# Optimization experiments

Measured on AMD Instinct MI355X. Metric: run time of the kernel, lower is better.

Reference implementation:

```python
import jax, jax.numpy as jnp
import numpy as np

NUM_FEAT = 64
K = 3  # dynamic kernel size
B, T, H, W = 1, 10, 192, 192


def _conv3x3(x, w, b):
    # x: [B,Cin,H,W], w: [Cout,Cin,3,3], b: [Cout]
    y = jax.lax.conv_general_dilated(x, w, window_strides=(1, 1), padding='SAME',
                                     dimension_numbers=('NCHW', 'OIHW', 'NCHW'))
    return y + b[None, :, None, None]


def _lrelu(x):
    return jnp.where(x >= 0, x, 0.1 * x)


def _kernel_conv(feat, core):
    # Per-pixel dynamic 3x3 filtering (CDVD-TSPNL KernelConv, sep_conv=False, no bias, N=1).
    # feat: [B,C,H,W], core: [B, K*K*C, H, W] -> out: [B,C,H,W]
    b, c, h, w = feat.shape
    pad = jnp.pad(feat, ((0, 0), (0, 0), (1, 1), (1, 1)))
    # 9 shifted copies, kernel-index kk = i*K + j matches core.view(b,1,K*K,c,h,w) layout
    stack = jnp.stack([pad[:, :, i:i + h, j:j + w] for i in range(K) for j in range(K)], axis=1)  # [B,9,C,H,W]
    core = core.reshape(b, K * K, c, h, w)
    return jnp.sum(core * stack, axis=1)  # sum over kernel taps; mean over N=1 frames is identity


def setup_inputs() -> dict:
    key = jax.random.key(0)
    ks = jax.random.split(key, 8)
    s = 0.02  # keep recurrent magnitudes stable
    nf = NUM_FEAT
    return {
        'feature': jax.random.normal(ks[0], (B, T, nf, H, W), jnp.float32),
        'w_kc1': jax.random.normal(ks[1], (nf, 2 * nf, 3, 3), jnp.float32) * s,
        'b_kc1': jnp.zeros((nf,), jnp.float32),
        'w_kc2': jax.random.normal(ks[2], (K * K * nf, nf, 3, 3), jnp.float32) * s,
        'b_kc2': jnp.zeros((K * K * nf,), jnp.float32),
        'w_c1': jax.random.normal(ks[3], (2 * nf, 2 * nf, 3, 3), jnp.float32) * s,
        'b_c1': jnp.zeros((2 * nf,), jnp.float32),
        'w_c2': jax.random.normal(ks[4], (nf, nf, 3, 3), jnp.float32) * s,
        'b_c2': jnp.zeros((nf,), jnp.float32),
        'w_c3': jax.random.normal(ks[5], (nf, nf, 3, 3), jnp.float32) * s,
        'b_c3': jnp.zeros((nf,), jnp.float32),
    }


def reference(feature, w_kc1, b_kc1, w_kc2, b_kc2, w_c1, b_c1, w_c2, b_c2, w_c3, b_c3):
    b, t, c, h, w = feature.shape
    feat_prop = feature[:, t - 1]  # [B,C,H,W]
    outs = [feat_prop]
    for i in range(t - 2, -1, -1):
        x_feat = feature[:, i]
        feat_concat = jnp.concatenate([x_feat, feat_prop], axis=1)
        kernel_predict = _conv3x3(_lrelu(_conv3x3(feat_concat, w_kc1, b_kc1)), w_kc2, b_kc2)
        feat_prop = _kernel_conv(feat_prop, kernel_predict)
        feat_fusion = _lrelu(_conv3x3(jnp.concatenate([x_feat, feat_prop], axis=1), w_c1, b_c1))
        p1, p2 = feat_fusion[:, :c], feat_fusion[:, c:]
        p1 = p1 * jax.nn.sigmoid(_conv3x3(p1, w_c2, b_c2))
        p2 = p2 * jax.nn.sigmoid(_conv3x3(p2, w_c3, b_c3))
        feat_prop = p1 + p2
        outs.append(feat_prop)
    return jnp.stack(outs[::-1], axis=1)  # [B,T,C,H,W]
```

## Files before the change

kernel.cpp:

```cpp
#include <hip/hip_runtime.h>

#define HH 192
#define WW 192
#define PW 194
#define HWSZ (HH*WW)
#define PHW (PW*PW)
#define CHW (64*HWSZ)

typedef __attribute__((ext_vector_type(8))) short bf16x8;
typedef __attribute__((ext_vector_type(4))) short bf16x4;
typedef __attribute__((ext_vector_type(4))) float f32x4;
typedef __attribute__((ext_vector_type(4))) unsigned int u32x4;

typedef __attribute__((address_space(3))) void as3_void;
typedef __attribute__((address_space(1))) const void as1_cvoid;

__device__ __forceinline__ float bf2f(short h) {
    union { unsigned u; float f; } c; c.u = ((unsigned)(unsigned short)h) << 16; return c.f;
}
__device__ __forceinline__ short f2bf(float f) {
    union { float f; unsigned u; } c; c.f = f;
    unsigned u = c.u;
    return (short)((u + 0x7FFFu + ((u >> 16) & 1u)) >> 16);
}
__device__ __forceinline__ float sigm(float v) {
    return 1.f / (1.f + __expf(-v));
}

template<int COUT>
__device__ __forceinline__ void stagew(short* lds, const short* wt, int kb, int mt,
                                       int tid, int wv)
{
    const short* wbase = wt + ((size_t)(kb*9)*COUT + mt*64)*64;
#pragma unroll
    for (int i = 0; i < 18; ++i) {
        int q = i*256 + tid;
        const short* gp = wbase + (size_t)(q >> 9)*COUT*64 + (q & 511)*8;
        __builtin_amdgcn_global_load_lds((as1_cvoid*)gp,
            (as3_void*)(lds + (i*256 + wv*64)*8), 16, 0, 0);
    }
}

template<int KB, int COUT>
__global__ __launch_bounds__(256, 2)
void convk(const short* __restrict__ in0, int cs0, int cb0,
           const short* __restrict__ in1, int cs1, int cb1,
           const short* __restrict__ wt, const float* __restrict__ bias,
           short* __restrict__ outb, int pado, int rowW, int cdst, int lrelu)
{
    __shared__ __align__(16) short lds[9*64*64];
    const int tid = threadIdx.x;
    const int l  = tid & 63, wv = tid >> 6;
    const int lr = l & 15,  lg = l >> 4;
    const int y  = blockIdx.x % HH;
    const int mt = blockIdx.x / HH;

    f32x4 acc[4][3];
#pragma unroll
    for (int a = 0; a < 4; ++a)
#pragma unroll
        for (int b = 0; b < 3; ++b) acc[a][b] = f32x4{0.f,0.f,0.f,0.f};

#pragma unroll 1
    for (int kb = 0; kb < KB; ++kb) {
        const short* src = (kb == 0) ? in0 : in1;
        const int cs = (kb == 0) ? cs0 : cs1;
        const int cb = (kb == 0) ? cb0 : cb1;
        if (kb) __syncthreads();
        stagew<COUT>(lds, wt, kb, mt, tid, wv);
        __syncthreads();
#pragma unroll
        for (int dy = 0; dy < 3; ++dy)
#pragma unroll
        for (int dx = 0; dx < 3; ++dx) {
            const int tap = dy*3 + dx;
#pragma unroll
            for (int ks = 0; ks < 2; ++ks) {
                bf16x8 bv[3];
#pragma unroll
                for (int nf = 0; nf < 3; ++nf) {
                    int px = wv*48 + nf*16 + lr + dx;
                    bv[nf] = *reinterpret_cast<const bf16x8*>(
                        src + (size_t)((y+dy)*PW + px)*cs + cb + ks*32 + lg*8);
                }
                const int s = ks*4 + lg;
#pragma unroll
                for (int mf = 0; mf < 4; ++mf) {
                    int row = mf*16 + lr;
                    bf16x8 av = *reinterpret_cast<const bf16x8*>(
                        &lds[(tap*64 + row)*64 + ((s ^ (row & 7))*8)]);
                    acc[mf][0] = __builtin_amdgcn_mfma_f32_16x16x32_bf16(av, bv[0], acc[mf][0], 0,0,0);
                    acc[mf][1] = __builtin_amdgcn_mfma_f32_16x16x32_bf16(av, bv[1], acc[mf][1], 0,0,0);
                    acc[mf][2] = __builtin_amdgcn_mfma_f32_16x16x32_bf16(av, bv[2], acc[mf][2], 0,0,0);
                }
            }
        }
    }

#pragma unroll
    for (int mf = 0; mf < 4; ++mf) {
        const int coutb = mt*64 + mf*16 + lg*4;
        f32x4 bv = *reinterpret_cast<const f32x4*>(bias + coutb);
#pragma unroll
        for (int nf = 0; nf < 3; ++nf) {
            const int x = wv*48 + nf*16 + lr;
            bf16x4 pk;
#pragma unroll
            for (int j = 0; j < 4; ++j) {
                float t = acc[mf][nf][j] + bv[j];
                if (lrelu) t = (t >= 0.f) ? t : 0.1f*t;
                pk[j] = f2bf(t);
            }
            *reinterpret_cast<bf16x4*>(outb + (size_t)((y+pado)*rowW + (x+pado))*cdst + coutb) = pk;
        }
    }
}

__global__ __launch_bounds__(256, 2)
void gatek(const short* __restrict__ fus, const short* __restrict__ wg,
           const float* __restrict__ b2, const float* __restrict__ b3,
           float* __restrict__ dml, short* __restrict__ fpst)
{
    __shared__ __align__(16) short lds[9*64*64];
    const int tid = threadIdx.x;
    const int l  = tid & 63, wv = tid >> 6;
    const int lr = l & 15,  lg = l >> 4;
    const int y  = blockIdx.x;

    f32x4 acc1[4][3], acc2[4][3];
#pragma unroll
    for (int a = 0; a < 4; ++a)
#pragma unroll
        for (int b = 0; b < 3; ++b) { acc1[a][b] = f32x4{0.f,0.f,0.f,0.f}; acc2[a][b] = f32x4{0.f,0.f,0.f,0.f}; }

#pragma unroll 1
    for (int g = 0; g < 2; ++g) {
        if (g) __syncthreads();
        stagew<64>(lds, wg + (size_t)g*9*64*64, 0, 0, tid, wv);
        __syncthreads();
#pragma unroll
        for (int dy = 0; dy < 3; ++dy)
#pragma unroll
        for (int dx = 0; dx < 3; ++dx) {
            const int tap = dy*3 + dx;
#pragma unroll
            for (int ks = 0; ks < 2; ++ks) {
                bf16x8 bv[3];
#pragma unroll
                for (int nf = 0; nf < 3; ++nf) {
                    int px = wv*48 + nf*16 + lr + dx;
                    bv[nf] = *reinterpret_cast<const bf16x8*>(
                        fus + (size_t)((y+dy)*PW + px)*128 + g*64 + ks*32 + lg*8);
                }
                const int s = ks*4 + lg;
#pragma unroll
                for (int mf = 0; mf < 4; ++mf) {
                    int row = mf*16 + lr;
                    bf16x8 av = *reinterpret_cast<const bf16x8*>(
                        &lds[(tap*64 + row)*64 + ((s ^ (row & 7))*8)]);
                    f32x4* ac = g ? &acc2[mf][0] : &acc1[mf][0];
                    ac[0] = __builtin_amdgcn_mfma_f32_16x16x32_bf16(av, bv[0], ac[0], 0,0,0);
                    ac[1] = __builtin_amdgcn_mfma_f32_16x16x32_bf16(av, bv[1], ac[1], 0,0,0);
                    ac[2] = __builtin_amdgcn_mfma_f32_16x16x32_bf16(av, bv[2], ac[2], 0,0,0);
                }
            }
        }
    }

#pragma unroll
    for (int mf = 0; mf < 4; ++mf) {
        const int c = mf*16 + lg*4;
        f32x4 v2 = *reinterpret_cast<const f32x4*>(b2 + c);
        f32x4 v3 = *reinterpret_cast<const f32x4*>(b3 + c);
#pragma unroll
        for (int nf = 0; nf < 3; ++nf) {
            const int x = wv*48 + nf*16 + lr;
            bf16x4 p1 = *reinterpret_cast<const bf16x4*>(fus + (size_t)((y+1)*PW + (x+1))*128 + c);
            bf16x4 p2 = *reinterpret_cast<const bf16x4*>(fus + (size_t)((y+1)*PW + (x+1))*128 + 64 + c);
            bf16x4 pk;
#pragma unroll
            for (int j = 0; j < 4; ++j) {
                float r = bf2f(p1[j]) * sigm(acc1[mf][nf][j] + v2[j])
                        + bf2f(p2[j]) * sigm(acc2[mf][nf][j] + v3[j]);
                dml[(size_t)(c + j)*HWSZ + y*WW + x] = r;
                pk[j] = f2bf(r);
            }
            *reinterpret_cast<bf16x4*>(fpst + (size_t)((y+1)*PW + (x+1))*64 + c) = pk;
        }
    }
}

__global__ __launch_bounds__(256)
void kconvk(const short* __restrict__ kp, const short* __restrict__ fp,
            short* __restrict__ outp)
{
    int t  = blockIdx.x*256 + threadIdx.x;
    int cg = t & 7, pix = t >> 3;
    int y = pix / WW, x = pix - y*WW;
    float acc[8];
#pragma unroll
    for (int e = 0; e < 8; ++e) acc[e] = 0.f;
    const short* kpp = kp + (size_t)pix*576 + cg*8;
#pragma unroll
    for (int tap = 0; tap < 9; ++tap) {
        int dy = tap / 3, dx = tap - dy*3;
        bf16x8 kv = *reinterpret_cast<const bf16x8*>(kpp + tap*64);
        bf16x8 fv = *reinterpret_cast<const bf16x8*>(fp + (size_t)((y+dy)*PW + (x+dx))*64 + cg*8);
#pragma unroll
        for (int e = 0; e < 8; ++e) acc[e] += bf2f(kv[e]) * bf2f(fv[e]);
    }
    bf16x8 o;
#pragma unroll
    for (int e = 0; e < 8; ++e) o[e] = f2bf(acc[e]);
    *reinterpret_cast<bf16x8*>(outp + (size_t)((y+1)*PW + (x+1))*64 + cg*8) = o;
}

__global__ __launch_bounds__(64)
void tonhwck(const float* __restrict__ src, short* __restrict__ dst)
{
    int b = blockIdx.x;
    int y = b / 3, x = (b - y*3)*64 + threadIdx.x;
    unsigned pk[32];
#pragma unroll
    for (int c = 0; c < 64; ++c) {
        unsigned h = (unsigned)(unsigned short)f2bf(src[(size_t)c*HWSZ + y*WW + x]);
        if (c & 1) pk[c>>1] |= h << 16; else pk[c>>1] = h;
    }
    u32x4* d = reinterpret_cast<u32x4*>(dst + (size_t)((y+1)*PW + (x+1))*64);
#pragma unroll
    for (int q = 0; q < 8; ++q) d[q] = u32x4{pk[4*q], pk[4*q+1], pk[4*q+2], pk[4*q+3]};
}

__global__ void wtxk(const float* __restrict__ src, short* __restrict__ dst,
                     int cout_n, int cin_n)
{
    int i = blockIdx.x*256 + threadIdx.x;
    if (i >= cout_n*cin_n) return;
    int co = i / cin_n, ci = i - co*cin_n;
    int kb = ci >> 6, cl = ci & 63, s = cl >> 3, e = cl & 7;
    const float* sp = src + (size_t)i*9;
    size_t base = ((size_t)(kb*9)*cout_n + co)*64 + ((s ^ (co & 7))*8) + e;
#pragma unroll
    for (int t = 0; t < 9; ++t)
        dst[base + (size_t)t*cout_n*64] = f2bf(sp[t]);
}

extern "C" void kernel_launch(void* const* d_in, const int* in_sizes, int n_in,
                              void* d_out, int out_size, void* d_ws, size_t ws_size,
                              hipStream_t stream)
{
    const float* feature = (const float*)d_in[0];
    const float* w_kc1 = (const float*)d_in[1];
    const float* b_kc1 = (const float*)d_in[2];
    const float* w_kc2 = (const float*)d_in[3];
    const float* b_kc2 = (const float*)d_in[4];
    const float* w_c1  = (const float*)d_in[5];
    const float* b_c1  = (const float*)d_in[6];
    const float* w_c2  = (const float*)d_in[7];
    const float* b_c2  = (const float*)d_in[8];
    const float* w_c3  = (const float*)d_in[9];
    const float* b_c3  = (const float*)d_in[10];
    float* out = (float*)d_out;
    char* ws = (char*)d_ws;

    size_t off = 0;
    auto alloc = [&](size_t bytes) -> void* {
        void* p = ws + off; off += (bytes + 255) & ~(size_t)255; return p;
    };
    short* wt1   = (short*)alloc((size_t)2*9*64*64*2);
    short* wt2   = (short*)alloc((size_t)9*576*64*2);
    short* wtc1  = (short*)alloc((size_t)2*9*128*64*2);
    short* wg    = (short*)alloc((size_t)2*9*64*64*2);
    char*  zbase = ws + off;
    short* featX   = (short*)alloc((size_t)PHW*64*2);
    short* fpinit  = (short*)alloc((size_t)PHW*64*2);
    short* fpstate = (short*)alloc((size_t)PHW*64*2);
    short* t1      = (short*)alloc((size_t)PHW*64*2);
    short* fpmid   = (short*)alloc((size_t)PHW*64*2);
    short* fusion  = (short*)alloc((size_t)PHW*128*2);
    size_t zbytes = (size_t)((ws + off) - zbase);
    short* kp   = (short*)alloc((size_t)HWSZ*576*2);
    (void)ws_size; (void)in_sizes; (void)n_in; (void)out_size;

    hipMemsetAsync(zbase, 0, zbytes, stream);
    wtxk<<<(64*128 + 255)/256, 256, 0, stream>>>(w_kc1, wt1, 64, 128);
    wtxk<<<(576*64 + 255)/256, 256, 0, stream>>>(w_kc2, wt2, 576, 64);
    wtxk<<<(128*128 + 255)/256, 256, 0, stream>>>(w_c1, wtc1, 128, 128);
    wtxk<<<(64*64 + 255)/256, 256, 0, stream>>>(w_c2, wg, 64, 64);
    wtxk<<<(64*64 + 255)/256, 256, 0, stream>>>(w_c3, wg + (size_t)9*64*64, 64, 64);
    tonhwck<<<576, 64, 0, stream>>>(feature + (size_t)9*CHW, fpinit);

    for (int i = 8; i >= 0; --i) {
        const short* fpin = (i == 8) ? fpinit : fpstate;
        tonhwck<<<576, 64, 0, stream>>>(feature + (size_t)i*CHW, featX);
        convk<2, 64><<<HH, 256, 0, stream>>>(featX, 64, 0, fpin, 64, 0,
            wt1, b_kc1, t1, 1, PW, 64, 1);
        convk<1, 576><<<9*HH, 256, 0, stream>>>(t1, 64, 0, nullptr, 0, 0,
            wt2, b_kc2, kp, 0, WW, 576, 0);
        kconvk<<<1152, 256, 0, stream>>>(kp, fpin, fpmid);
        convk<2, 128><<<2*HH, 256, 0, stream>>>(featX, 64, 0, fpmid, 64, 0,
            wtc1, b_c1, fusion, 1, PW, 128, 1);
        gatek<<<HH, 256, 0, stream>>>(fusion, wg, b_c2, b_c3,
            out + (size_t)i*CHW, fpstate);
    }
    hipMemcpyAsync(out + (size_t)9*CHW, feature + (size_t)9*CHW,
                   (size_t)CHW*sizeof(float), hipMemcpyDeviceToDevice, stream);
}
```

Before: 1.525 ms.

## Use 512-thread blocks covering two rows for kernel-predict conv, remap rows into bands

The large 576-output-channel conv now uses 512-thread blocks where 8 waves cover two image rows, so each staged 64-channel weight tile in LDS is reused across twice as many pixels and weight staging traffic halves. Block indices are also remapped so consecutive blocks interleave across 8 row bands, which may spread work more evenly across XCDs and their caches. The larger blocks raise per-block register and occupancy pressure under launch_bounds(512,2).

```diff
diff --git a/kernel.cpp b/kernel.cpp
--- a/kernel.cpp
+++ b/kernel.cpp
@@ -27,22 +27,22 @@
     return 1.f / (1.f + __expf(-v));
 }
 
-template<int COUT>
+template<int COUT, int TPB>
 __device__ __forceinline__ void stagew(short* lds, const short* wt, int kb, int mt,
                                        int tid, int wv)
 {
     const short* wbase = wt + ((size_t)(kb*9)*COUT + mt*64)*64;
 #pragma unroll
-    for (int i = 0; i < 18; ++i) {
-        int q = i*256 + tid;
+    for (int i = 0; i < 4608/TPB; ++i) {
+        int q = i*TPB + tid;
         const short* gp = wbase + (size_t)(q >> 9)*COUT*64 + (q & 511)*8;
         __builtin_amdgcn_global_load_lds((as1_cvoid*)gp,
-            (as3_void*)(lds + (i*256 + wv*64)*8), 16, 0, 0);
-    }
-}
-
-template<int KB, int COUT>
-__global__ __launch_bounds__(256, 2)
+            (as3_void*)(lds + (i*TPB + wv*64)*8), 16, 0, 0);
+    }
+}
+
+template<int KB, int COUT, int TPB>
+__global__ __launch_bounds__(TPB, 2)
 void convk(const short* __restrict__ in0, int cs0, int cb0,
            const short* __restrict__ in1, int cs1, int cb1,
            const short* __restrict__ wt, const float* __restrict__ bias,
@@ -52,8 +52,19 @@
     const int tid = threadIdx.x;
     const int l  = tid & 63, wv = tid >> 6;
     const int lr = l & 15,  lg = l >> 4;
-    const int y  = blockIdx.x % HH;
-    const int mt = blockIdx.x / HH;
+    const int band = blockIdx.x & 7;
+    const int j    = blockIdx.x >> 3;
+    int mt, y, x0;
+    if constexpr (TPB == 512) {
+        mt = j / 12;
+        int yp = band*12 + (j - mt*12);
+        y = yp*2 + (wv >> 2);
+        x0 = (wv & 3)*48;
+    } else {
+        mt = j / 24;
+        y = band*24 + (j - mt*24);
+        x0 = wv*48;
+    }
 
     f32x4 acc[4][3];
 #pragma unroll
@@ -67,7 +78,7 @@
         const int cs = (kb == 0) ? cs0 : cs1;
         const int cb = (kb == 0) ? cb0 : cb1;
         if (kb) __syncthreads();
-        stagew<COUT>(lds, wt, kb, mt, tid, wv);
+        stagew<COUT, TPB>(lds, wt, kb, mt, tid, wv);
         __syncthreads();
 #pragma unroll
         for (int dy = 0; dy < 3; ++dy)
@@ -79,7 +90,7 @@
                 bf16x8 bv[3];
 #pragma unroll
                 for (int nf = 0; nf < 3; ++nf) {
-                    int px = wv*48 + nf*16 + lr + dx;
+                    int px = x0 + nf*16 + lr + dx;
                     bv[nf] = *reinterpret_cast<const bf16x8*>(
                         src + (size_t)((y+dy)*PW + px)*cs + cb + ks*32 + lg*8);
                 }
@@ -103,13 +114,13 @@
         f32x4 bv = *reinterpret_cast<const f32x4*>(bias + coutb);
 #pragma unroll
         for (int nf = 0; nf < 3; ++nf) {
-            const int x = wv*48 + nf*16 + lr;
+            const int x = x0 + nf*16 + lr;
             bf16x4 pk;
 #pragma unroll
-            for (int j = 0; j < 4; ++j) {
-                float t = acc[mf][nf][j] + bv[j];
+            for (int j2 = 0; j2 < 4; ++j2) {
+                float t = acc[mf][nf][j2] + bv[j2];
                 if (lrelu) t = (t >= 0.f) ? t : 0.1f*t;
-                pk[j] = f2bf(t);
+                pk[j2] = f2bf(t);
             }
             *reinterpret_cast<bf16x4*>(outb + (size_t)((y+pado)*rowW + (x+pado))*cdst + coutb) = pk;
         }
@@ -125,7 +136,7 @@
     const int tid = threadIdx.x;
     const int l  = tid & 63, wv = tid >> 6;
     const int lr = l & 15,  lg = l >> 4;
-    const int y  = blockIdx.x;
+    const int y  = (blockIdx.x & 7)*24 + (blockIdx.x >> 3);
 
     f32x4 acc1[4][3], acc2[4][3];
 #pragma unroll
@@ -136,7 +147,7 @@
 #pragma unroll 1
     for (int g = 0; g < 2; ++g) {
         if (g) __syncthreads();
-        stagew<64>(lds, wg + (size_t)g*9*64*64, 0, 0, tid, wv);
+        stagew<64, 256>(lds, wg + (size_t)g*9*64*64, 0, 0, tid, wv);
         __syncthreads();
 #pragma unroll
         for (int dy = 0; dy < 3; ++dy)
@@ -293,12 +304,12 @@
     for (int i = 8; i >= 0; --i) {
         const short* fpin = (i == 8) ? fpinit : fpstate;
         tonhwck<<<576, 64, 0, stream>>>(feature + (size_t)i*CHW, featX);
-        convk<2, 64><<<HH, 256, 0, stream>>>(featX, 64, 0, fpin, 64, 0,
+        convk<2, 64, 256><<<HH, 256, 0, stream>>>(featX, 64, 0, fpin, 64, 0,
             wt1, b_kc1, t1, 1, PW, 64, 1);
-        convk<1, 576><<<9*HH, 256, 0, stream>>>(t1, 64, 0, nullptr, 0, 0,
+        convk<1, 576, 512><<<9*96, 512, 0, stream>>>(t1, 64, 0, nullptr, 0, 0,
             wt2, b_kc2, kp, 0, WW, 576, 0);
         kconvk<<<1152, 256, 0, stream>>>(kp, fpin, fpmid);
-        convk<2, 128><<<2*HH, 256, 0, stream>>>(featX, 64, 0, fpmid, 64, 0,
+        convk<2, 128, 256><<<2*HH, 256, 0, stream>>>(featX, 64, 0, fpmid, 64, 0,
             wtc1, b_c1, fusion, 1, PW, 128, 1);
         gatek<<<HH, 256, 0, stream>>>(fusion, wg, b_c2, b_c3,
             out + (size_t)i*CHW, fpstate);
```

New measurement: 1.564 ms. +2.5%, slower.
